# Performance work log

Measured on AMD Instinct MI355X. Metric: run time of the kernel, lower is better.

Reference implementation:

```python
import jax, jax.numpy as jnp
import numpy as np

B, H, N, D = 4, 8, 2048, 64

def setup_inputs() -> dict:
    key = jax.random.key(0)
    kq, kk, kv = jax.random.split(key, 3)
    q = jax.random.uniform(kq, (B, H, N, D), dtype=jnp.float32)
    k = jax.random.uniform(kk, (B, H, N, D), dtype=jnp.float32)
    v = jax.random.normal(kv, (B, H, N, D), dtype=jnp.float32)
    return {"q": q, "k": k, "v": v}

def reference(q, k, v):
    d = k.shape[-1]
    # Hamming-similarity score: 0.5 * (1 + (2q-1)(2k-1)^T / d)
    sim = jnp.einsum("bhnd,bhmd->bhnm", 2.0 * q - 1.0, 2.0 * k - 1.0)
    score = jax.nn.softmax(0.5 * (1.0 + sim / d), axis=-1)
    out = jnp.einsum("bhnm,bhmd->bhnd", score, v)
    return (out, score)
```

## Files before the change

kernel.cpp:

```cpp
#include <hip/hip_runtime.h>
#include <hip/hip_bf16.h>

#define NN 2048
#define DD 64
#define BHH 32

typedef __attribute__((ext_vector_type(8))) short bf16x8;
typedef __attribute__((ext_vector_type(4))) float f32x4;

__device__ __forceinline__ unsigned short f2b(float f) {
    __hip_bfloat16 h = __float2bfloat16(f);
    return __builtin_bit_cast(unsigned short, h);
}

__global__ void prep_qk(const float4* __restrict__ q, const float4* __restrict__ k,
                        ushort4* __restrict__ qo, ushort4* __restrict__ ko) {
    int i = blockIdx.x * 256 + threadIdx.x;
    float4 a = q[i], b = k[i];
    ushort4 qa, kb;
    qa.x = f2b(2.f*a.x - 1.f); qa.y = f2b(2.f*a.y - 1.f);
    qa.z = f2b(2.f*a.z - 1.f); qa.w = f2b(2.f*a.w - 1.f);
    kb.x = f2b(2.f*b.x - 1.f); kb.y = f2b(2.f*b.y - 1.f);
    kb.z = f2b(2.f*b.z - 1.f); kb.w = f2b(2.f*b.w - 1.f);
    qo[i] = qa; ko[i] = kb;
}

__global__ void prep_v(const float* __restrict__ v, unsigned short* __restrict__ vt) {
    __shared__ float tile[64][65];
    int bh = blockIdx.x >> 5, jt = blockIdx.x & 31;
    int t = threadIdx.x;
    const float* src = v + ((size_t)bh * NN + jt * 64) * DD;
#pragma unroll
    for (int h = 0; h < 4; ++h) {
        int cc = t + h * 256;
        int row = cc >> 4, c4 = cc & 15;
        float4 f = *(const float4*)(src + row * DD + c4 * 4);
        tile[row][c4*4+0] = f.x; tile[row][c4*4+1] = f.y;
        tile[row][c4*4+2] = f.z; tile[row][c4*4+3] = f.w;
    }
    __syncthreads();
    unsigned short* dst = vt + (size_t)bh * DD * NN + jt * 64;
#pragma unroll
    for (int h = 0; h < 2; ++h) {
        int cc = t + h * 256;
        int d = cc >> 3, c8 = cc & 7;
        unsigned int w0 = (unsigned)f2b(tile[c8*8+0][d]) | ((unsigned)f2b(tile[c8*8+1][d]) << 16);
        unsigned int w1 = (unsigned)f2b(tile[c8*8+2][d]) | ((unsigned)f2b(tile[c8*8+3][d]) << 16);
        unsigned int w2 = (unsigned)f2b(tile[c8*8+4][d]) | ((unsigned)f2b(tile[c8*8+5][d]) << 16);
        unsigned int w3 = (unsigned)f2b(tile[c8*8+6][d]) | ((unsigned)f2b(tile[c8*8+7][d]) << 16);
        uint4 pk = { w0, w1, w2, w3 };
        *(uint4*)(dst + (size_t)d * NN + c8 * 8) = pk;
    }
}

__device__ __forceinline__ void stage_tile(unsigned short (*dst)[72],
                                           const unsigned short* __restrict__ src,
                                           int srcStride, int tid) {
#pragma unroll
    for (int h = 0; h < 2; ++h) {
        int cc = tid + h * 256;
        int row = cc >> 3, c8 = cc & 7;
        uint4 val = *(const uint4*)(src + (size_t)row * srcStride + c8 * 8);
        *(uint4*)&dst[row][c8 * 8] = val;
    }
}

__global__ __launch_bounds__(256, 4) void attn(
        const unsigned short* __restrict__ Qw, const unsigned short* __restrict__ Kw,
        const unsigned short* __restrict__ Vtw,
        float* __restrict__ outp, float* __restrict__ score) {
    __shared__ unsigned short qa[64][72], kb[64][72], vt[64][72], pl[64][72];
    __shared__ float lsum[64];

    int tid = threadIdx.x;
    int bh = blockIdx.x & 31, qt = blockIdx.x >> 5;
    int i0 = qt * 64;
    const unsigned short* Qh = Qw + ((size_t)bh * NN + i0) * DD;
    const unsigned short* Kh = Kw + (size_t)bh * NN * DD;
    const unsigned short* Vh = Vtw + (size_t)bh * DD * NN;
    float* scoreH = score + (size_t)bh * NN * NN + (size_t)i0 * NN;
    float* outH   = outp  + ((size_t)bh * NN + i0) * DD;

    int lane = tid & 63, wave = tid >> 6;
    int l4 = lane & 15, quad = lane >> 4;
    int row0 = wave * 16;

    stage_tile(qa, Qh, DD, tid);

    float psum[4] = {0.f, 0.f, 0.f, 0.f};
    for (int kt = 0; kt < 32; ++kt) {
        __syncthreads();
        stage_tile(kb, Kh + (size_t)kt * 64 * DD, DD, tid);
        __syncthreads();
        bf16x8 a0 = *(const bf16x8*)&qa[row0 + l4][quad * 8];
        bf16x8 a1 = *(const bf16x8*)&qa[row0 + l4][32 + quad * 8];
#pragma unroll
        for (int nb = 0; nb < 4; ++nb) {
            bf16x8 b0 = *(const bf16x8*)&kb[nb * 16 + l4][quad * 8];
            bf16x8 b1 = *(const bf16x8*)&kb[nb * 16 + l4][32 + quad * 8];
            f32x4 acc = {0.f, 0.f, 0.f, 0.f};
            acc = __builtin_amdgcn_mfma_f32_16x16x32_bf16(a0, b0, acc, 0, 0, 0);
            acc = __builtin_amdgcn_mfma_f32_16x16x32_bf16(a1, b1, acc, 0, 0, 0);
#pragma unroll
            for (int r = 0; r < 4; ++r)
                psum[r] += __expf(fmaf(acc[r], 0.0078125f, 0.5f));
        }
    }
#pragma unroll
    for (int r = 0; r < 4; ++r) {
#pragma unroll
        for (int m = 1; m < 16; m <<= 1) psum[r] += __shfl_xor(psum[r], m, 64);
    }
    if (l4 == 0) {
#pragma unroll
        for (int r = 0; r < 4; ++r) lsum[row0 + quad * 4 + r] = psum[r];
    }
    __syncthreads();
    float rinv[4];
#pragma unroll
    for (int r = 0; r < 4; ++r) rinv[r] = 1.0f / lsum[row0 + quad * 4 + r];

    f32x4 o[4];
#pragma unroll
    for (int nb = 0; nb < 4; ++nb) o[nb] = (f32x4){0.f, 0.f, 0.f, 0.f};

    for (int kt = 0; kt < 32; ++kt) {
        __syncthreads();
        stage_tile(kb, Kh + (size_t)kt * 64 * DD, DD, tid);
        stage_tile(vt, Vh + kt * 64, NN, tid);
        __syncthreads();
        bf16x8 a0 = *(const bf16x8*)&qa[row0 + l4][quad * 8];
        bf16x8 a1 = *(const bf16x8*)&qa[row0 + l4][32 + quad * 8];
#pragma unroll
        for (int nb = 0; nb < 4; ++nb) {
            bf16x8 b0 = *(const bf16x8*)&kb[nb * 16 + l4][quad * 8];
            bf16x8 b1 = *(const bf16x8*)&kb[nb * 16 + l4][32 + quad * 8];
            f32x4 acc = {0.f, 0.f, 0.f, 0.f};
            acc = __builtin_amdgcn_mfma_f32_16x16x32_bf16(a0, b0, acc, 0, 0, 0);
            acc = __builtin_amdgcn_mfma_f32_16x16x32_bf16(a1, b1, acc, 0, 0, 0);
#pragma unroll
            for (int r = 0; r < 4; ++r) {
                float p = __expf(fmaf(acc[r], 0.0078125f, 0.5f)) * rinv[r];
                int rr = row0 + quad * 4 + r;
                __builtin_nontemporal_store(p, &scoreH[(size_t)rr * NN + kt * 64 + nb * 16 + l4]);
                pl[rr][nb * 16 + l4] = f2b(p);
            }
        }
        __syncthreads();
        bf16x8 p0 = *(const bf16x8*)&pl[row0 + l4][quad * 8];
        bf16x8 p1 = *(const bf16x8*)&pl[row0 + l4][32 + quad * 8];
#pragma unroll
        for (int nb = 0; nb < 4; ++nb) {
            bf16x8 v0 = *(const bf16x8*)&vt[nb * 16 + l4][quad * 8];
            bf16x8 v1 = *(const bf16x8*)&vt[nb * 16 + l4][32 + quad * 8];
            o[nb] = __builtin_amdgcn_mfma_f32_16x16x32_bf16(p0, v0, o[nb], 0, 0, 0);
            o[nb] = __builtin_amdgcn_mfma_f32_16x16x32_bf16(p1, v1, o[nb], 0, 0, 0);
        }
    }
#pragma unroll
    for (int nb = 0; nb < 4; ++nb) {
#pragma unroll
        for (int r = 0; r < 4; ++r)
            outH[(size_t)(row0 + quad * 4 + r) * DD + nb * 16 + l4] = o[nb][r];
    }
}

extern "C" void kernel_launch(void* const* d_in, const int* in_sizes, int n_in,
                              void* d_out, int out_size, void* d_ws, size_t ws_size,
                              hipStream_t stream) {
    const float* q = (const float*)d_in[0];
    const float* k = (const float*)d_in[1];
    const float* v = (const float*)d_in[2];
    float* outp  = (float*)d_out;
    float* score = outp + (size_t)4 * 8 * 2048 * 64;

    unsigned short* Qw  = (unsigned short*)d_ws;
    unsigned short* Kw  = Qw + (size_t)4 * 8 * 2048 * 64;
    unsigned short* Vtw = Kw + (size_t)4 * 8 * 2048 * 64;

    prep_qk<<<4096, 256, 0, stream>>>((const float4*)q, (const float4*)k,
                                      (ushort4*)Qw, (ushort4*)Kw);
    prep_v<<<1024, 256, 0, stream>>>(v, Vtw);
    attn<<<1024, 256, 0, stream>>>(Qw, Kw, Vtw, outp, score);
}
```

Baseline: 731.9 us.

## Double-buffer K/V tiles and stage score writes through LDS as vector stores

The attention kernel now double-buffers K and V tiles in shared memory, prefetching the next tile into registers so global loads overlap with MFMA work and only one barrier is needed per iteration. Score probabilities are written to a per-wave LDS tile and then emitted as 16-byte nontemporal vector stores, replacing scattered 4-byte stores. The P operand for the PV matmul is built from that same tile, which drops a separate bf16 buffer and its barrier. Each block now handles two query tiles with Q kept in registers, the grid is halved and launch bounds drop to 2 blocks per CU, so occupancy may fall.

After: 635.4 us. -13.2%, faster.

```diff
diff --git a/kernel.cpp b/kernel.cpp
--- a/kernel.cpp
+++ b/kernel.cpp
@@ -3,7 +3,6 @@
 
 #define NN 2048
 #define DD 64
-#define BHH 32
 
 typedef __attribute__((ext_vector_type(8))) short bf16x8;
 typedef __attribute__((ext_vector_type(4))) float f32x4;
@@ -53,115 +52,187 @@
     }
 }
 
-__device__ __forceinline__ void stage_tile(unsigned short (*dst)[72],
-                                           const unsigned short* __restrict__ src,
-                                           int srcStride, int tid) {
-#pragma unroll
-    for (int h = 0; h < 2; ++h) {
-        int cc = tid + h * 256;
-        int row = cc >> 3, c8 = cc & 7;
-        uint4 val = *(const uint4*)(src + (size_t)row * srcStride + c8 * 8);
-        *(uint4*)&dst[row][c8 * 8] = val;
-    }
-}
-
-__global__ __launch_bounds__(256, 4) void attn(
+__global__ __launch_bounds__(256, 2) void attn(
         const unsigned short* __restrict__ Qw, const unsigned short* __restrict__ Kw,
         const unsigned short* __restrict__ Vtw,
         float* __restrict__ outp, float* __restrict__ score) {
-    __shared__ unsigned short qa[64][72], kb[64][72], vt[64][72], pl[64][72];
+    __shared__ unsigned short kb[2][64][72];
+    __shared__ unsigned short vt[2][64][72];
+    __shared__ float sc[4][16][68];
     __shared__ float lsum[64];
 
-    int tid = threadIdx.x;
-    int bh = blockIdx.x & 31, qt = blockIdx.x >> 5;
-    int i0 = qt * 64;
-    const unsigned short* Qh = Qw + ((size_t)bh * NN + i0) * DD;
+    const int tid = threadIdx.x;
+    const int bh = blockIdx.x & 31, qp = blockIdx.x >> 5;
+    const int lane = tid & 63, wave = tid >> 6;
+    const int l4 = lane & 15, quad = lane >> 4;
+    const int row0 = wave * 16;
+
     const unsigned short* Kh = Kw + (size_t)bh * NN * DD;
     const unsigned short* Vh = Vtw + (size_t)bh * DD * NN;
-    float* scoreH = score + (size_t)bh * NN * NN + (size_t)i0 * NN;
-    float* outH   = outp  + ((size_t)bh * NN + i0) * DD;
-
-    int lane = tid & 63, wave = tid >> 6;
-    int l4 = lane & 15, quad = lane >> 4;
-    int row0 = wave * 16;
-
-    stage_tile(qa, Qh, DD, tid);
-
-    float psum[4] = {0.f, 0.f, 0.f, 0.f};
-    for (int kt = 0; kt < 32; ++kt) {
-        __syncthreads();
-        stage_tile(kb, Kh + (size_t)kt * 64 * DD, DD, tid);
-        __syncthreads();
-        bf16x8 a0 = *(const bf16x8*)&qa[row0 + l4][quad * 8];
-        bf16x8 a1 = *(const bf16x8*)&qa[row0 + l4][32 + quad * 8];
-#pragma unroll
-        for (int nb = 0; nb < 4; ++nb) {
-            bf16x8 b0 = *(const bf16x8*)&kb[nb * 16 + l4][quad * 8];
-            bf16x8 b1 = *(const bf16x8*)&kb[nb * 16 + l4][32 + quad * 8];
-            f32x4 acc = {0.f, 0.f, 0.f, 0.f};
-            acc = __builtin_amdgcn_mfma_f32_16x16x32_bf16(a0, b0, acc, 0, 0, 0);
-            acc = __builtin_amdgcn_mfma_f32_16x16x32_bf16(a1, b1, acc, 0, 0, 0);
+
+    const int sr0 = tid >> 3,         sc0 = (tid & 7) * 8;
+    const int sr1 = (tid + 256) >> 3, sc1 = ((tid + 256) & 7) * 8;
+
+    for (int it = 0; it < 2; ++it) {
+        const int i0 = (qp * 2 + it) * 64;
+        const unsigned short* Qh = Qw + ((size_t)bh * NN + i0) * DD;
+        float* scoreH = score + (size_t)bh * NN * NN + (size_t)i0 * NN;
+        float* outH   = outp  + ((size_t)bh * NN + i0) * DD;
+
+        {
+            uint4 t0 = *(const uint4*)(Qh + (size_t)sr0 * DD + sc0);
+            uint4 t1 = *(const uint4*)(Qh + (size_t)sr1 * DD + sc1);
+            *(uint4*)&kb[0][sr0][sc0] = t0;
+            *(uint4*)&kb[0][sr1][sc1] = t1;
+        }
+        __syncthreads();
+        const bf16x8 a0 = *(const bf16x8*)&kb[0][row0 + l4][quad * 8];
+        const bf16x8 a1 = *(const bf16x8*)&kb[0][row0 + l4][32 + quad * 8];
+        __syncthreads();
+
+        uint4 k0 = *(const uint4*)(Kh + (size_t)sr0 * DD + sc0);
+        uint4 k1 = *(const uint4*)(Kh + (size_t)sr1 * DD + sc1);
+        *(uint4*)&kb[0][sr0][sc0] = k0;
+        *(uint4*)&kb[0][sr1][sc1] = k1;
+        k0 = *(const uint4*)(Kh + (size_t)64 * DD + (size_t)sr0 * DD + sc0);
+        k1 = *(const uint4*)(Kh + (size_t)64 * DD + (size_t)sr1 * DD + sc1);
+        __syncthreads();
+
+        float psum[4] = {0.f, 0.f, 0.f, 0.f};
+        for (int kt = 0; kt < 32; ++kt) {
+            const int cur = kt & 1, nxt = cur ^ 1;
+            if (kt + 1 < 32) {
+                *(uint4*)&kb[nxt][sr0][sc0] = k0;
+                *(uint4*)&kb[nxt][sr1][sc1] = k1;
+            }
+            if (kt + 2 < 32) {
+                const unsigned short* s = Kh + (size_t)(kt + 2) * 64 * DD;
+                k0 = *(const uint4*)(s + (size_t)sr0 * DD + sc0);
+                k1 = *(const uint4*)(s + (size_t)sr1 * DD + sc1);
+            }
+#pragma unroll
+            for (int nb = 0; nb < 4; ++nb) {
+                bf16x8 b0 = *(const bf16x8*)&kb[cur][nb * 16 + l4][quad * 8];
+                bf16x8 b1 = *(const bf16x8*)&kb[cur][nb * 16 + l4][32 + quad * 8];
+                f32x4 acc = {0.f, 0.f, 0.f, 0.f};
+                acc = __builtin_amdgcn_mfma_f32_16x16x32_bf16(a0, b0, acc, 0, 0, 0);
+                acc = __builtin_amdgcn_mfma_f32_16x16x32_bf16(a1, b1, acc, 0, 0, 0);
+#pragma unroll
+                for (int r = 0; r < 4; ++r)
+                    psum[r] += __expf(fmaf(acc[r], 0.0078125f, 0.5f));
+            }
+            __syncthreads();
+        }
+#pragma unroll
+        for (int r = 0; r < 4; ++r) {
+#pragma unroll
+            for (int m = 1; m < 16; m <<= 1) psum[r] += __shfl_xor(psum[r], m, 64);
+        }
+        if (l4 == 0) {
+#pragma unroll
+            for (int r = 0; r < 4; ++r) lsum[row0 + quad * 4 + r] = psum[r];
+        }
+
+        uint4 w0, w1;
+        k0 = *(const uint4*)(Kh + (size_t)sr0 * DD + sc0);
+        k1 = *(const uint4*)(Kh + (size_t)sr1 * DD + sc1);
+        w0 = *(const uint4*)(Vh + (size_t)sr0 * NN + sc0);
+        w1 = *(const uint4*)(Vh + (size_t)sr1 * NN + sc1);
+        *(uint4*)&kb[0][sr0][sc0] = k0;
+        *(uint4*)&kb[0][sr1][sc1] = k1;
+        *(uint4*)&vt[0][sr0][sc0] = w0;
+        *(uint4*)&vt[0][sr1][sc1] = w1;
+        k0 = *(const uint4*)(Kh + (size_t)64 * DD + (size_t)sr0 * DD + sc0);
+        k1 = *(const uint4*)(Kh + (size_t)64 * DD + (size_t)sr1 * DD + sc1);
+        w0 = *(const uint4*)(Vh + 64 + (size_t)sr0 * NN + sc0);
+        w1 = *(const uint4*)(Vh + 64 + (size_t)sr1 * NN + sc1);
+        __syncthreads();
+
+        float rinv[4];
+#pragma unroll
+        for (int r = 0; r < 4; ++r) rinv[r] = 1.0f / lsum[row0 + quad * 4 + r];
+        f32x4 o[4];
+#pragma unroll
+        for (int nb = 0; nb < 4; ++nb) o[nb] = (f32x4){0.f, 0.f, 0.f, 0.f};
+
+        for (int kt = 0; kt < 32; ++kt) {
+            const int cur = kt & 1, nxt = cur ^ 1;
+            if (kt > 0) {
+#pragma unroll
+                for (int h = 0; h < 4; ++h) {
+                    const int rr = h * 4 + quad;
+                    f32x4 wv = *(const f32x4*)&sc[wave][rr][l4 * 4];
+                    __builtin_nontemporal_store(wv,
+                        (f32x4*)&scoreH[(size_t)(row0 + rr) * NN + (kt - 1) * 64 + l4 * 4]);
+                }
+            }
+            if (kt + 1 < 32) {
+                *(uint4*)&kb[nxt][sr0][sc0] = k0;
+                *(uint4*)&kb[nxt][sr1][sc1] = k1;
+                *(uint4*)&vt[nxt][sr0][sc0] = w0;
+                *(uint4*)&vt[nxt][sr1][sc1] = w1;
+            }
+            if (kt + 2 < 32) {
+                const unsigned short* sk = Kh + (size_t)(kt + 2) * 64 * DD;
+                const unsigned short* sv = Vh + (size_t)(kt + 2) * 64;
+                k0 = *(const uint4*)(sk + (size_t)sr0 * DD + sc0);
+                k1 = *(const uint4*)(sk + (size_t)sr1 * DD + sc1);
+                w0 = *(const uint4*)(sv + (size_t)sr0 * NN + sc0);
+                w1 = *(const uint4*)(sv + (size_t)sr1 * NN + sc1);
+            }
+#pragma unroll
+            for (int nb = 0; nb < 4; ++nb) {
+                bf16x8 b0 = *(const bf16x8*)&kb[cur][nb * 16 + l4][quad * 8];
+                bf16x8 b1 = *(const bf16x8*)&kb[cur][nb * 16 + l4][32 + quad * 8];
+                f32x4 acc = {0.f, 0.f, 0.f, 0.f};
+                acc = __builtin_amdgcn_mfma_f32_16x16x32_bf16(a0, b0, acc, 0, 0, 0);
+                acc = __builtin_amdgcn_mfma_f32_16x16x32_bf16(a1, b1, acc, 0, 0, 0);
+#pragma unroll
+                for (int r = 0; r < 4; ++r) {
+                    float p = __expf(fmaf(acc[r], 0.0078125f, 0.5f)) * rinv[r];
+                    sc[wave][quad * 4 + r][nb * 16 + l4] = p;
+                }
+            }
+            f32x4 x0 = *(const f32x4*)&sc[wave][l4][quad * 8];
+            f32x4 x1 = *(const f32x4*)&sc[wave][l4][quad * 8 + 4];
+            f32x4 y0 = *(const f32x4*)&sc[wave][l4][32 + quad * 8];
+            f32x4 y1 = *(const f32x4*)&sc[wave][l4][32 + quad * 8 + 4];
+            bf16x8 p0, p1;
+#pragma unroll
+            for (int j = 0; j < 4; ++j) {
+                p0[j]     = (short)f2b(x0[j]);
+                p0[j + 4] = (short)f2b(x1[j]);
+                p1[j]     = (short)f2b(y0[j]);
+                p1[j + 4] = (short)f2b(y1[j]);
+            }
+#pragma unroll
+            for (int nb = 0; nb < 4; ++nb) {
+                bf16x8 u0 = *(const bf16x8*)&vt[cur][nb * 16 + l4][quad * 8];
+                bf16x8 u1 = *(const bf16x8*)&vt[cur][nb * 16 + l4][32 + quad * 8];
+                o[nb] = __builtin_amdgcn_mfma_f32_16x16x32_bf16(p0, u0, o[nb], 0, 0, 0);
+                o[nb] = __builtin_amdgcn_mfma_f32_16x16x32_bf16(p1, u1, o[nb], 0, 0, 0);
+            }
+            __syncthreads();
+        }
+#pragma unroll
+        for (int h = 0; h < 4; ++h) {
+            const int rr = h * 4 + quad;
+            f32x4 wv = *(const f32x4*)&sc[wave][rr][l4 * 4];
+            __builtin_nontemporal_store(wv,
+                (f32x4*)&scoreH[(size_t)(row0 + rr) * NN + 31 * 64 + l4 * 4]);
+        }
+#pragma unroll
+        for (int nb = 0; nb < 4; ++nb)
 #pragma unroll
             for (int r = 0; r < 4; ++r)
-                psum[r] += __expf(fmaf(acc[r], 0.0078125f, 0.5f));
-        }
-    }
-#pragma unroll
-    for (int r = 0; r < 4; ++r) {
-#pragma unroll
-        for (int m = 1; m < 16; m <<= 1) psum[r] += __shfl_xor(psum[r], m, 64);
-    }
-    if (l4 == 0) {
-#pragma unroll
-        for (int r = 0; r < 4; ++r) lsum[row0 + quad * 4 + r] = psum[r];
-    }
-    __syncthreads();
-    float rinv[4];
-#pragma unroll
-    for (int r = 0; r < 4; ++r) rinv[r] = 1.0f / lsum[row0 + quad * 4 + r];
-
-    f32x4 o[4];
-#pragma unroll
-    for (int nb = 0; nb < 4; ++nb) o[nb] = (f32x4){0.f, 0.f, 0.f, 0.f};
-
-    for (int kt = 0; kt < 32; ++kt) {
-        __syncthreads();
-        stage_tile(kb, Kh + (size_t)kt * 64 * DD, DD, tid);
-        stage_tile(vt, Vh + kt * 64, NN, tid);
-        __syncthreads();
-        bf16x8 a0 = *(const bf16x8*)&qa[row0 + l4][quad * 8];
-        bf16x8 a1 = *(const bf16x8*)&qa[row0 + l4][32 + quad * 8];
-#pragma unroll
-        for (int nb = 0; nb < 4; ++nb) {
-            bf16x8 b0 = *(const bf16x8*)&kb[nb * 16 + l4][quad * 8];
-            bf16x8 b1 = *(const bf16x8*)&kb[nb * 16 + l4][32 + quad * 8];
-            f32x4 acc = {0.f, 0.f, 0.f, 0.f};
-            acc = __builtin_amdgcn_mfma_f32_16x16x32_bf16(a0, b0, acc, 0, 0, 0);
-            acc = __builtin_amdgcn_mfma_f32_16x16x32_bf16(a1, b1, acc, 0, 0, 0);
-#pragma unroll
-            for (int r = 0; r < 4; ++r) {
-                float p = __expf(fmaf(acc[r], 0.0078125f, 0.5f)) * rinv[r];
-                int rr = row0 + quad * 4 + r;
-                __builtin_nontemporal_store(p, &scoreH[(size_t)rr * NN + kt * 64 + nb * 16 + l4]);
-                pl[rr][nb * 16 + l4] = f2b(p);
-            }
-        }
-        __syncthreads();
-        bf16x8 p0 = *(const bf16x8*)&pl[row0 + l4][quad * 8];
-        bf16x8 p1 = *(const bf16x8*)&pl[row0 + l4][32 + quad * 8];
-#pragma unroll
-        for (int nb = 0; nb < 4; ++nb) {
-            bf16x8 v0 = *(const bf16x8*)&vt[nb * 16 + l4][quad * 8];
-            bf16x8 v1 = *(const bf16x8*)&vt[nb * 16 + l4][32 + quad * 8];
-            o[nb] = __builtin_amdgcn_mfma_f32_16x16x32_bf16(p0, v0, o[nb], 0, 0, 0);
-            o[nb] = __builtin_amdgcn_mfma_f32_16x16x32_bf16(p1, v1, o[nb], 0, 0, 0);
-        }
-    }
-#pragma unroll
-    for (int nb = 0; nb < 4; ++nb) {
-#pragma unroll
-        for (int r = 0; r < 4; ++r)
-            outH[(size_t)(row0 + quad * 4 + r) * DD + nb * 16 + l4] = o[nb][r];
+                sc[wave][quad * 4 + r][nb * 16 + l4] = o[nb][r];
+#pragma unroll
+        for (int h = 0; h < 4; ++h) {
+            const int rr = h * 4 + quad;
+            f32x4 wv = *(const f32x4*)&sc[wave][rr][l4 * 4];
+            *(f32x4*)&outH[(size_t)(row0 + rr) * DD + l4 * 4] = wv;
+        }
+        __syncthreads();
     }
 }
 
@@ -181,5 +252,5 @@
     prep_qk<<<4096, 256, 0, stream>>>((const float4*)q, (const float4*)k,
                                       (ushort4*)Qw, (ushort4*)Kw);
     prep_v<<<1024, 256, 0, stream>>>(v, Vtw);
-    attn<<<1024, 256, 0, stream>>>(Qw, Kw, Vtw, outp, score);
-}
+    attn<<<512, 256, 0, stream>>>(Qw, Kw, Vtw, outp, score);
+}
```
